# Performance work log

Measured on AMD Instinct MI355X. Metric: run time of the kernel, lower is better.

The kernel has to match this reference:

```python
import jax, jax.numpy as jnp
import numpy as np

# --- constants from init_kwargs ---
ANCHORS = np.array([1.3221, 1.73145, 3.19275, 4.00944, 5.05587,
                    8.09892, 9.47112, 4.84053, 11.2364, 10.0071], np.float32).reshape(5, 2)
NA = 5           # num_anchors
NC = 1           # num_classes (per meta input)
CS = 20          # meta classes (target.size(1))
MAX_BOXES = 50
COORD_SCALE = 1.0
NOOBJ_SCALE = 1.0
OBJ_SCALE = 5.0
CLASS_SCALE = 1.0
SIL_THRESH = 0.6
N_META = 20      # enews buckets


def _iou(cx1, cy1, w1, h1, cx2, cy2, w2, h2):
    # center-format IoU, matching bbox_ious(..., x1y1x2y2=False)
    mx = jnp.minimum(cx1 - 0.5 * w1, cx2 - 0.5 * w2)
    Mx = jnp.maximum(cx1 + 0.5 * w1, cx2 + 0.5 * w2)
    my = jnp.minimum(cy1 - 0.5 * h1, cy2 - 0.5 * h2)
    My = jnp.maximum(cy1 + 0.5 * h1, cy2 + 0.5 * h2)
    cw = w1 + w2 - (Mx - mx)
    ch = h1 + h2 - (My - my)
    inter = jnp.where((cw > 0) & (ch > 0), cw * ch, 0.0)
    return inter / (w1 * h1 + w2 * h2 - inter)


def setup_inputs() -> dict:
    key = jax.random.key(0)
    k1, k2, k3, k4 = jax.random.split(key, 4)
    output = jax.random.normal(k1, (320, 30, 26, 26), dtype=jnp.float32)
    target = jax.random.uniform(k2, (16, 20, 250), dtype=jnp.float32)
    dynamic_weights = jax.random.normal(k3, (1, 64, 1024), dtype=jnp.float32)
    target_cls_ids = jax.random.randint(k4, (64,), 0, 20, dtype=jnp.int32)
    return {"output": output, "target": target,
            "dynamic_weights": dynamic_weights, "target_cls_ids": target_cls_ids}


def reference(output, target, dynamic_weights, target_cls_ids):
    target = jax.lax.stop_gradient(target)  # torch uses target.data
    dw = dynamic_weights[0]                 # (n_dw, D)

    nB, ch, nH, nW = output.shape
    bs = nB // CS
    K = NA * nH * nW
    out5 = output.reshape(nB, NA, 5 + NC, nH, nW)
    x = jax.nn.sigmoid(out5[:, :, 0])
    y = jax.nn.sigmoid(out5[:, :, 1])
    w = out5[:, :, 2]
    h = out5[:, :, 3]
    conf = jax.nn.sigmoid(out5[:, :, 4])
    # meta classification logits: softmax across the cs meta inputs
    cls_logits = out5[:, :, 5].reshape(bs, CS, K)  # nC == 1

    aw = jnp.asarray(ANCHORS[:, 0])
    ah = jnp.asarray(ANCHORS[:, 1])
    grid_x = jnp.arange(nW, dtype=jnp.float32)
    grid_y = jnp.arange(nH, dtype=jnp.float32)

    # decoded pred boxes (torch builds them from .data -> detached)
    px = jax.lax.stop_gradient(x) + grid_x[None, None, None, :]
    py = jax.lax.stop_gradient(y) + grid_y[None, None, :, None]
    pw = jnp.exp(jax.lax.stop_gradient(w)) * aw[None, :, None, None]
    ph = jnp.exp(jax.lax.stop_gradient(h)) * ah[None, :, None, None]

    # ---- build_targets (vectorized) ----
    g = target.reshape(nB, MAX_BOXES, 5)
    valid = g[:, :, 1] != 0
    gxs = g[:, :, 1] * nW
    gys = g[:, :, 2] * nH
    gws = g[:, :, 3] * nW
    ghs = g[:, :, 4] * nH

    pb = lambda t: t.reshape(nB, K, 1)
    ious = _iou(pb(px), pb(py), pb(pw), pb(ph),
                gxs[:, None, :], gys[:, None, :], gws[:, None, :], ghs[:, None, :])  # (nB,K,50)
    cur_ious = jnp.max(jnp.where(valid[:, None, :], ious, 0.0), axis=-1)
    conf_mask = jnp.where(cur_ious > SIL_THRESH, 0.0, NOOBJ_SCALE).reshape(nB, NA, nH, nW)

    # seen < 12800 branch (self.seen = 0)
    shape4 = (nB, NA, nH, nW)
    coord_mask = jnp.ones(shape4, jnp.float32)
    tx = jnp.full(shape4, 0.5, jnp.float32)
    ty = jnp.full(shape4, 0.5, jnp.float32)
    tw = jnp.zeros(shape4, jnp.float32)
    th = jnp.zeros(shape4, jnp.float32)
    tconf = jnp.zeros(shape4, jnp.float32)
    cls_mask = jnp.zeros(shape4, jnp.float32)

    # best anchor per gt by wh-IoU (anchor_step == 2)
    inter_a = jnp.minimum(gws[..., None], aw) * jnp.minimum(ghs[..., None], ah)
    iou_a = inter_a / (gws[..., None] * ghs[..., None] + aw * ah - inter_a)
    best_n = jnp.argmax(iou_a, axis=-1)  # (nB,50)

    gi = jnp.clip(gxs.astype(jnp.int32), 0, nW - 1)
    gj = jnp.clip(gys.astype(jnp.int32), 0, nH - 1)
    b_idx = jnp.broadcast_to(jnp.arange(nB)[:, None], (nB, MAX_BOXES))
    fidx = ((b_idx * NA + best_n) * nH + gj) * nW + gi
    fidx = jnp.where(valid, fidx, nB * NA * nH * nW).reshape(-1)  # OOB -> dropped

    def scat(base, vals):
        return base.reshape(-1).at[fidx].set(vals.reshape(-1), mode='drop').reshape(shape4)

    pbx = px[b_idx, best_n, gj, gi]
    pby = py[b_idx, best_n, gj, gi]
    pbw = pw[b_idx, best_n, gj, gi]
    pbh = ph[b_idx, best_n, gj, gi]
    iou_gt = _iou(gxs, gys, gws, ghs, pbx, pby, pbw, pbh)

    ones = jnp.ones_like(gxs)
    coord_mask = scat(coord_mask, ones)
    cls_mask = scat(cls_mask, ones)
    conf_mask = scat(conf_mask, jnp.full_like(gxs, OBJ_SCALE))
    tx = scat(tx, gxs - gi.astype(jnp.float32))
    ty = scat(ty, gys - gj.astype(jnp.float32))
    tw = scat(tw, jnp.log(gws / aw[best_n]))
    th = scat(th, jnp.log(ghs / ah[best_n]))
    tconf = scat(tconf, iou_gt)

    # ---- region losses ----
    loss_x = COORD_SCALE * 0.5 * jnp.sum(coord_mask * (x - tx) ** 2)
    loss_y = COORD_SCALE * 0.5 * jnp.sum(coord_mask * (y - ty) ** 2)
    loss_w = COORD_SCALE * 0.5 * jnp.sum(coord_mask * (w - tw) ** 2)
    loss_h = COORD_SCALE * 0.5 * jnp.sum(coord_mask * (h - th) ** 2)
    loss_conf = 0.5 * jnp.sum(conf_mask * (conf - tconf) ** 2)

    logp = jax.nn.log_softmax(jnp.transpose(cls_logits, (0, 2, 1)), axis=-1)  # (bs,K,CS)
    mask_bc = cls_mask.reshape(bs, CS, K)
    loss_cls = CLASS_SCALE * (-jnp.sum(mask_bc * jnp.transpose(logp, (0, 2, 1))))

    # ---- max-margin term over dynamic reweighting vectors ----
    cnt = jax.ops.segment_sum(jnp.ones(dw.shape[0], jnp.float32), target_cls_ids, N_META)
    sums = jax.ops.segment_sum(dw, target_cls_ids, N_META)
    enews = sums / jnp.maximum(cnt, 1.0)[:, None]
    present = cnt > 0
    same = jnp.sum((dw - enews[target_cls_ids]) ** 2)
    d = jnp.sum((enews[:, None, :] - enews[None, :, :]) ** 2, axis=-1)
    vp = present[:, None] & present[None, :] & (~jnp.eye(N_META, dtype=bool))
    dmin = jnp.min(jnp.where(vp, d, jnp.inf), axis=1)
    different = jnp.sum(jnp.where(jnp.any(vp, axis=1), dmin, 0.0))

    return loss_x + loss_y + loss_w + loss_h + loss_conf + loss_cls + same - different
```

## Files before the change

### kernel.cpp

```cpp
#include <hip/hip_runtime.h>
#include <math.h>

#define NB 320
#define NAC 5
#define NH 26
#define NW 26
#define CHW 676
#define KTOT 3380
#define BSTRIDE 20280
#define MAXB 50
#define CS 20
#define NMETA 20
#define DWROWS 64
#define DWDIM 1024
#define NPAIR (NMETA * NMETA)
#define NCBLK 2
#define NPARTR (NB * NCBLK)
#define NSAMEPAIR (NMETA + NPAIR)
#define NMETAY ((NSAMEPAIR + NCBLK - 1) / NCBLK)
#define NPART (NPARTR + NMETA)

__constant__ float c_aw[5] = {1.3221f, 3.19275f, 5.05587f, 9.47112f, 11.2364f};
__constant__ float c_ah[5] = {1.73145f, 4.00944f, 8.09892f, 4.84053f, 10.0071f};

__device__ __forceinline__ float rl_f(float v, int l) {
    return __int_as_float(__builtin_amdgcn_readlane(__float_as_int(v), l));
}

__global__ __launch_bounds__(256) void fused_k(const float* __restrict__ out,
                                               const float* __restrict__ target,
                                               const float* __restrict__ dw,
                                               const int* __restrict__ ids,
                                               float* __restrict__ part,
                                               float* __restrict__ dmat) {
    __shared__ float sred[4];
    __shared__ float4 sbox[MAXB];
    __shared__ float sta[MAXB];
    int tid = threadIdx.x;
    int lane = tid & 63;
    int wid = tid >> 6;
    int b = blockIdx.y;

    if (b >= NB) {
        int p = (b - NB) * NCBLK + blockIdx.x;
        float s = 0.0f;
        if (p < NMETA) {
            int c = p;
            float acc[4] = {0, 0, 0, 0}, ssq[4] = {0, 0, 0, 0};
            int cnt = 0;
            for (int r = 0; r < DWROWS; r++) {
                int idr = ids[r];
                if (idr == c) {
                    cnt++;
#pragma unroll
                    for (int k = 0; k < 4; k++) {
                        float v = dw[r * DWDIM + tid + k * 256];
                        acc[k] += v; ssq[k] += v * v;
                    }
                }
            }
            if (cnt > 0) {
                float inv = 1.0f / (float)cnt;
#pragma unroll
                for (int k = 0; k < 4; k++) {
                    float e = acc[k] * inv;
                    s += ssq[k] - (float)cnt * e * e;
                }
            }
        } else if (p < NSAMEPAIR) {
            int pp = p - NMETA;
            int pi = pp / NMETA, pj = pp - pi * NMETA;
            if (pi != pj) {
                float ai[4] = {0, 0, 0, 0}, aj[4] = {0, 0, 0, 0};
                int ci = 0, cj = 0;
                for (int r = 0; r < DWROWS; r++) {
                    int idr = ids[r];
                    if (idr == pi) {
                        ci++;
#pragma unroll
                        for (int k = 0; k < 4; k++) ai[k] += dw[r * DWDIM + tid + k * 256];
                    } else if (idr == pj) {
                        cj++;
#pragma unroll
                        for (int k = 0; k < 4; k++) aj[k] += dw[r * DWDIM + tid + k * 256];
                    }
                }
                float ii = 1.0f / fmaxf((float)ci, 1.0f);
                float ij = 1.0f / fmaxf((float)cj, 1.0f);
#pragma unroll
                for (int k = 0; k < 4; k++) {
                    float df = ai[k] * ii - aj[k] * ij;
                    s += df * df;
                }
            }
        }
#pragma unroll
        for (int o = 32; o > 0; o >>= 1) s += __shfl_down(s, o, 64);
        if (lane == 0) sred[wid] = s;
        __syncthreads();
        if (tid == 0 && p < NSAMEPAIR) {
            float tot = sred[0] + sred[1] + sred[2] + sred[3];
            if (p < NMETA) part[NPARTR + p] = tot;
            else dmat[p - NMETA] = tot;
        }
        return;
    }

    if (tid < MAXB) {
        const float* g = target + b * (MAXB * 5) + tid * 5;
        float g1 = g[1];
        float gx = g1 * (float)NW;
        float gy = g[2] * (float)NH;
        float gw = g[3] * (float)NW;
        float gh = g[4] * (float)NH;
        float4 e;
        float ta;
        if (g1 != 0.0f) {
            e.x = gx - 0.5f * gw; e.y = gx + 0.5f * gw;
            e.z = gy - 0.5f * gh; e.w = gy + 0.5f * gh;
            ta = 0.375f * gw * gh;
        } else {
            e.x = 1e30f; e.y = -1e30f; e.z = 1e30f; e.w = -1e30f;
            ta = 0.0f;
        }
        sbox[tid] = e;
        sta[tid] = ta;
    }
    __syncthreads();

    bool isbox = (blockIdx.x == NCBLK - 1) && (wid == 3);
    float contrib = 0.0f;

    if (!isbox) {
        int k0 = blockIdx.x * 2048 + tid * 8;
        float PLOX[8], PHIX[8], PLOY[8], PHIY[8], THR[8], CF[8], SM[8];
        int ng = 0;
#pragma unroll
        for (int g4 = 0; g4 < 2; g4++) {
            int kg = k0 + g4 * 4;
            if (kg < KTOT) {
                int a = kg / CHW;
                int rem0 = kg - a * CHW;
                const float* base = out + (size_t)b * BSTRIDE + a * 6 * CHW + rem0;
                float4 R0 = *(const float4*)(base + 0 * CHW);
                float4 R1 = *(const float4*)(base + 1 * CHW);
                float4 R2 = *(const float4*)(base + 2 * CHW);
                float4 R3 = *(const float4*)(base + 3 * CHW);
                float4 R4 = *(const float4*)(base + 4 * CHW);
                float RX[4] = {R0.x, R0.y, R0.z, R0.w};
                float RY[4] = {R1.x, R1.y, R1.z, R1.w};
                float RW[4] = {R2.x, R2.y, R2.z, R2.w};
                float RH[4] = {R3.x, R3.y, R3.z, R3.w};
                float RC[4] = {R4.x, R4.y, R4.z, R4.w};
                float aw = c_aw[a], ah = c_ah[a];
#pragma unroll
                for (int c = 0; c < 4; c++) {
                    int rem = rem0 + c;
                    int i = rem / NW;
                    int j = rem - i * NW;
                    float x = 1.0f / (1.0f + __expf(-RX[c]));
                    float y = 1.0f / (1.0f + __expf(-RY[c]));
                    float conf = 1.0f / (1.0f + __expf(-RC[c]));
                    float pw = __expf(RW[c]) * aw;
                    float ph = __expf(RH[c]) * ah;
                    float px = x + (float)j;
                    float py = y + (float)i;
                    int q = ng + c;
                    PLOX[q] = px - 0.5f * pw; PHIX[q] = px + 0.5f * pw;
                    PLOY[q] = py - 0.5f * ph; PHIY[q] = py + 0.5f * ph;
                    THR[q] = 0.375f * (pw * ph);
                    SM[q] = -1e30f;
                    CF[q] = conf;
                    float dx = x - 0.5f, dy = y - 0.5f;
                    contrib += 0.5f * (dx * dx + dy * dy + RW[c] * RW[c] + RH[c] * RH[c]);
                }
                ng += 4;
            }
        }
        if (ng > 0) {
            for (int tb = 0; tb < MAXB; tb++) {
                float4 e = sbox[tb];
                float ta = sta[tb];
#pragma unroll
                for (int q = 0; q < 8; q++) {
                    if (q >= ng) break;
                    float ix = fminf(PHIX[q], e.y) - fmaxf(PLOX[q], e.x);
                    float iy = fminf(PHIY[q], e.w) - fmaxf(PLOY[q], e.z);
                    SM[q] = fmaxf(SM[q], __builtin_fmaf(fmaxf(ix, 0.0f), iy, -ta));
                }
            }
#pragma unroll
            for (int q = 0; q < 8; q++) {
                if (q >= ng) break;
                if (!(SM[q] > THR[q])) contrib += 0.5f * CF[q] * CF[q];
            }
        }
    } else {
        int t = lane;
        const float* g = target + b * (MAXB * 5) + ((t < MAXB) ? t : 0) * 5;
        float g1 = g[1];
        float gx = g1 * (float)NW;
        float gy = g[2] * (float)NH;
        float gw = g[3] * (float)NW;
        float gh = g[4] * (float)NH;
        bool bvalid = (g1 != 0.0f) && (t < MAXB);

        int fidx = -1 - t;
        int bn = 0, gi = 0, gj = 0;
        if (bvalid) {
            float area = gw * gh;
            float best = -1.0f;
#pragma unroll
            for (int n = 0; n < 5; n++) {
                float inter = fminf(gw, c_aw[n]) * fminf(gh, c_ah[n]);
                float iou = inter / (area + c_aw[n] * c_ah[n] - inter);
                if (iou > best) { best = iou; bn = n; }
            }
            gi = min(max((int)gx, 0), NW - 1);
            gj = min(max((int)gy, 0), NH - 1);
            fidx = (bn * NH + gj) * NW + gi;
        }
        bool winner = bvalid;
        for (int t2 = 1; t2 < MAXB; t2++) {
            int f2 = __builtin_amdgcn_readlane(fidx, t2);
            winner = winner && ((t2 <= t) || (f2 != fidx));
        }
        if (winner) {
            int rem = gj * NW + gi;
            const float* cell = out + (size_t)b * BSTRIDE + bn * 6 * CHW + rem;
            float rx = cell[0 * CHW];
            float ry = cell[1 * CHW];
            float w  = cell[2 * CHW];
            float h  = cell[3 * CHW];
            float rc = cell[4 * CHW];
            float x = 1.0f / (1.0f + __expf(-rx));
            float y = 1.0f / (1.0f + __expf(-ry));
            float conf = 1.0f / (1.0f + __expf(-rc));
            float aw = c_aw[bn], ah = c_ah[bn];
            float pw = __expf(w) * aw;
            float ph = __expf(h) * ah;
            float px = x + (float)gi;
            float py = y + (float)gj;
            float plox = px - 0.5f * pw, phix = px + 0.5f * pw;
            float ploy = py - 0.5f * ph, phiy = py + 0.5f * ph;
            float parea = pw * ph;
            float thr = 0.375f * parea;
            float smax = -1e30f;
            for (int tb = 0; tb < MAXB; tb++) {
                float4 e = sbox[tb];
                float ta = sta[tb];
                float ix = fminf(phix, e.y) - fmaxf(plox, e.x);
                float iy = fminf(phiy, e.w) - fmaxf(ploy, e.z);
                smax = fmaxf(smax, __builtin_fmaf(fmaxf(ix, 0.0f), iy, -ta));
            }
            bool silent = smax > thr;
            float dx0 = x - 0.5f, dy0 = y - 0.5f;
            float basel = 0.5f * (dx0 * dx0 + dy0 * dy0 + w * w + h * h);
            if (!silent) basel += 0.5f * conf * conf;
            float blox = gx - 0.5f * gw, bhix = gx + 0.5f * gw;
            float bloy = gy - 0.5f * gh, bhiy = gy + 0.5f * gh;
            float ix = fminf(phix, bhix) - fmaxf(plox, blox);
            float iy = fminf(phiy, bhiy) - fmaxf(ploy, bloy);
            float inter = fmaxf(ix, 0.0f) * fmaxf(iy, 0.0f);
            float iou = inter / (parea + gw * gh - inter);
            float txv = gx - (float)gi, tyv = gy - (float)gj;
            float twv = __logf(gw / aw), thv = __logf(gh / ah);
            float dx = x - txv, dy = y - tyv;
            float dwv = w - twv, dhv = h - thv;
            float dc = conf - iou;
            float ovr = 0.5f * (dx * dx + dy * dy + dwv * dwv + dhv * dhv) + 2.5f * dc * dc;
            int bs = b / CS, cs = b - bs * CS;
            const float* cl = out + (size_t)(bs * CS) * BSTRIDE + (bn * 6 + 5) * CHW + rem;
            float v[CS];
            float m = -1e30f;
#pragma unroll
            for (int c2 = 0; c2 < CS; c2++) { v[c2] = cl[(size_t)c2 * BSTRIDE]; m = fmaxf(m, v[c2]); }
            float s = 0.0f, own = 0.0f;
#pragma unroll
            for (int c2 = 0; c2 < CS; c2++) {
                s += __expf(v[c2] - m);
                if (c2 == cs) own = v[c2];
            }
            contrib = ovr - basel + (m + __logf(s)) - own;
        }
    }

#pragma unroll
    for (int o = 32; o > 0; o >>= 1) contrib += __shfl_down(contrib, o, 64);
    if (lane == 0) sred[wid] = contrib;
    __syncthreads();
    if (tid == 0) part[b * NCBLK + blockIdx.x] = sred[0] + sred[1] + sred[2] + sred[3];
}

__global__ __launch_bounds__(256) void finish_k(const int* __restrict__ ids,
                                                const float* __restrict__ part,
                                                const float* __restrict__ dmat,
                                                float* __restrict__ loss) {
    __shared__ float sred[4];
    __shared__ int scnt[NMETA];
    __shared__ float sdd;
    int tid = threadIdx.x;
    int lane = tid & 63, wid = tid >> 6;

    if (tid < NMETA) {
        int c = 0;
        for (int r = 0; r < DWROWS; r++) c += (ids[r] == tid) ? 1 : 0;
        scnt[tid] = c;
    }
    __syncthreads();
    float dd = 0.0f;
    if (tid < NMETA && scnt[tid] > 0) {
        float dmin = INFINITY;
        bool any = false;
        for (int j = 0; j < NMETA; j++) {
            if (j != tid && scnt[j] > 0) {
                any = true;
                dmin = fminf(dmin, dmat[tid * NMETA + j]);
            }
        }
        dd = any ? dmin : 0.0f;
    }
    if (tid < 64) {
#pragma unroll
        for (int o = 32; o > 0; o >>= 1) dd += __shfl_down(dd, o, 64);
        if (tid == 0) sdd = dd;
    }
    float ps = 0.0f;
    for (int i2 = tid; i2 < NPART; i2 += 256) ps += part[i2];
#pragma unroll
    for (int o = 32; o > 0; o >>= 1) ps += __shfl_down(ps, o, 64);
    if (lane == 0) sred[wid] = ps;
    __syncthreads();
    if (tid == 0) loss[0] = (sred[0] + sred[1] + sred[2] + sred[3]) - sdd;
}

extern "C" void kernel_launch(void* const* d_in, const int* in_sizes, int n_in,
                              void* d_out, int out_size, void* d_ws, size_t ws_size,
                              hipStream_t stream) {
    const float* output = (const float*)d_in[0];
    const float* target = (const float*)d_in[1];
    const float* dw     = (const float*)d_in[2];
    const int*   ids    = (const int*)d_in[3];
    float* loss = (float*)d_out;

    float* part = (float*)d_ws;
    float* dmat = part + NPART;

    dim3 grid(NCBLK, NB + NMETAY);
    fused_k<<<grid, 256, 0, stream>>>(output, target, dw, ids, part, dmat);
    finish_k<<<1, 256, 0, stream>>>(ids, part, dmat, loss);
}
```

Measured before the change: 109.4 us.

## Split each batch across four blocks with four cells per thread

Doubles the number of blocks per batch image so each thread handles four grid cells instead of eight. The box-scan loop also prefetches the next ground-truth box from shared memory. This is meant to raise occupancy and parallelism and to cut per-thread register pressure and serial work. In exchange, the per-block setup is done twice as often, there are more partial sums to reduce, and the box-matching warp moves to a different wave index.

```diff
diff --git a/kernel.cpp b/kernel.cpp
--- a/kernel.cpp
+++ b/kernel.cpp
@@ -14,7 +14,7 @@
 #define DWROWS 64
 #define DWDIM 1024
 #define NPAIR (NMETA * NMETA)
-#define NCBLK 2
+#define NCBLK 4
 #define NPARTR (NB * NCBLK)
 #define NSAMEPAIR (NMETA + NPAIR)
 #define NMETAY ((NSAMEPAIR + NCBLK - 1) / NCBLK)
@@ -128,71 +128,66 @@
     }
     __syncthreads();
 
-    bool isbox = (blockIdx.x == NCBLK - 1) && (wid == 3);
+    bool isbox = (blockIdx.x == NCBLK - 1) && (wid == 2);
     float contrib = 0.0f;
 
     if (!isbox) {
-        int k0 = blockIdx.x * 2048 + tid * 8;
-        float PLOX[8], PHIX[8], PLOY[8], PHIY[8], THR[8], CF[8], SM[8];
-        int ng = 0;
-#pragma unroll
-        for (int g4 = 0; g4 < 2; g4++) {
-            int kg = k0 + g4 * 4;
-            if (kg < KTOT) {
-                int a = kg / CHW;
-                int rem0 = kg - a * CHW;
-                const float* base = out + (size_t)b * BSTRIDE + a * 6 * CHW + rem0;
-                float4 R0 = *(const float4*)(base + 0 * CHW);
-                float4 R1 = *(const float4*)(base + 1 * CHW);
-                float4 R2 = *(const float4*)(base + 2 * CHW);
-                float4 R3 = *(const float4*)(base + 3 * CHW);
-                float4 R4 = *(const float4*)(base + 4 * CHW);
-                float RX[4] = {R0.x, R0.y, R0.z, R0.w};
-                float RY[4] = {R1.x, R1.y, R1.z, R1.w};
-                float RW[4] = {R2.x, R2.y, R2.z, R2.w};
-                float RH[4] = {R3.x, R3.y, R3.z, R3.w};
-                float RC[4] = {R4.x, R4.y, R4.z, R4.w};
-                float aw = c_aw[a], ah = c_ah[a];
+        int k0 = blockIdx.x * 1024 + tid * 4;
+        if (k0 < KTOT) {
+            int a = k0 / CHW;
+            int rem0 = k0 - a * CHW;
+            const float* base = out + (size_t)b * BSTRIDE + a * 6 * CHW + rem0;
+            float4 R0 = *(const float4*)(base + 0 * CHW);
+            float4 R1 = *(const float4*)(base + 1 * CHW);
+            float4 R2 = *(const float4*)(base + 2 * CHW);
+            float4 R3 = *(const float4*)(base + 3 * CHW);
+            float4 R4 = *(const float4*)(base + 4 * CHW);
+            float RX[4] = {R0.x, R0.y, R0.z, R0.w};
+            float RY[4] = {R1.x, R1.y, R1.z, R1.w};
+            float RW[4] = {R2.x, R2.y, R2.z, R2.w};
+            float RH[4] = {R3.x, R3.y, R3.z, R3.w};
+            float RC[4] = {R4.x, R4.y, R4.z, R4.w};
+            float CF[4];
+            float PLOX[4], PHIX[4], PLOY[4], PHIY[4], THR[4], SM[4];
+            float aw = c_aw[a], ah = c_ah[a];
+#pragma unroll
+            for (int c = 0; c < 4; c++) {
+                int rem = rem0 + c;
+                int i = rem / NW;
+                int j = rem - i * NW;
+                float x = 1.0f / (1.0f + __expf(-RX[c]));
+                float y = 1.0f / (1.0f + __expf(-RY[c]));
+                float conf = 1.0f / (1.0f + __expf(-RC[c]));
+                float pw = __expf(RW[c]) * aw;
+                float ph = __expf(RH[c]) * ah;
+                float px = x + (float)j;
+                float py = y + (float)i;
+                PLOX[c] = px - 0.5f * pw; PHIX[c] = px + 0.5f * pw;
+                PLOY[c] = py - 0.5f * ph; PHIY[c] = py + 0.5f * ph;
+                THR[c] = 0.375f * (pw * ph);
+                SM[c] = -1e30f;
+                CF[c] = conf;
+                float dx = x - 0.5f, dy = y - 0.5f;
+                contrib += 0.5f * (dx * dx + dy * dy + RW[c] * RW[c] + RH[c] * RH[c]);
+            }
+            float4 e = sbox[0];
+            float ta = sta[0];
+#pragma unroll 5
+            for (int tb = 0; tb < MAXB; tb++) {
+                int nxt = (tb + 1 < MAXB) ? tb + 1 : tb;
+                float4 en = sbox[nxt];
+                float tan_ = sta[nxt];
 #pragma unroll
                 for (int c = 0; c < 4; c++) {
-                    int rem = rem0 + c;
-                    int i = rem / NW;
-                    int j = rem - i * NW;
-                    float x = 1.0f / (1.0f + __expf(-RX[c]));
-                    float y = 1.0f / (1.0f + __expf(-RY[c]));
-                    float conf = 1.0f / (1.0f + __expf(-RC[c]));
-                    float pw = __expf(RW[c]) * aw;
-                    float ph = __expf(RH[c]) * ah;
-                    float px = x + (float)j;
-                    float py = y + (float)i;
-                    int q = ng + c;
-                    PLOX[q] = px - 0.5f * pw; PHIX[q] = px + 0.5f * pw;
-                    PLOY[q] = py - 0.5f * ph; PHIY[q] = py + 0.5f * ph;
-                    THR[q] = 0.375f * (pw * ph);
-                    SM[q] = -1e30f;
-                    CF[q] = conf;
-                    float dx = x - 0.5f, dy = y - 0.5f;
-                    contrib += 0.5f * (dx * dx + dy * dy + RW[c] * RW[c] + RH[c] * RH[c]);
-                }
-                ng += 4;
-            }
-        }
-        if (ng > 0) {
-            for (int tb = 0; tb < MAXB; tb++) {
-                float4 e = sbox[tb];
-                float ta = sta[tb];
-#pragma unroll
-                for (int q = 0; q < 8; q++) {
-                    if (q >= ng) break;
-                    float ix = fminf(PHIX[q], e.y) - fmaxf(PLOX[q], e.x);
-                    float iy = fminf(PHIY[q], e.w) - fmaxf(PLOY[q], e.z);
-                    SM[q] = fmaxf(SM[q], __builtin_fmaf(fmaxf(ix, 0.0f), iy, -ta));
-                }
-            }
-#pragma unroll
-            for (int q = 0; q < 8; q++) {
-                if (q >= ng) break;
-                if (!(SM[q] > THR[q])) contrib += 0.5f * CF[q] * CF[q];
+                    float ix = fminf(PHIX[c], e.y) - fmaxf(PLOX[c], e.x);
+                    float iy = fminf(PHIY[c], e.w) - fmaxf(PLOY[c], e.z);
+                    SM[c] = fmaxf(SM[c], __builtin_fmaf(fmaxf(ix, 0.0f), iy, -ta));
+                }
+                e = en; ta = tan_;
+            }
+#pragma unroll
+            for (int c = 0; c < 4; c++) {
+                if (!(SM[c] > THR[c])) contrib += 0.5f * CF[c] * CF[c];
             }
         }
     } else {
```

New measurement: 98.41 us. 10.1% less time.
